# Kernel tuning notes

Measured on AMD Instinct MI355X. Metric: run time of the kernel, lower is better.

The kernel has to match this reference:

```python
import jax, jax.numpy as jnp
import numpy as np

SCORE_THRESH = 0.05
NMS_THRESH = 0.5
MAX_DET = 100
BBOX_XFORM_CLIP = float(np.log(1000.0 / 16.0))


def decode_boxes(proposals, deltas):
    # proposals, deltas: [..., 4] in (x1, y1, x2, y2) / (dx, dy, dw, dh)
    w = proposals[..., 2] - proposals[..., 0]
    h = proposals[..., 3] - proposals[..., 1]
    cx = proposals[..., 0] + 0.5 * w
    cy = proposals[..., 1] + 0.5 * h
    dx, dy = deltas[..., 0], deltas[..., 1]
    dw = jnp.minimum(deltas[..., 2], BBOX_XFORM_CLIP)
    dh = jnp.minimum(deltas[..., 3], BBOX_XFORM_CLIP)
    pcx = dx * w + cx
    pcy = dy * h + cy
    pw = jnp.exp(dw) * w
    ph = jnp.exp(dh) * h
    return jnp.stack([pcx - 0.5 * pw, pcy - 0.5 * ph,
                      pcx + 0.5 * pw, pcy + 0.5 * ph], axis=-1)


def iou_matrix(boxes):
    # boxes: [N, 4] -> [N, N] pairwise IoU
    area = (boxes[:, 2] - boxes[:, 0]) * (boxes[:, 3] - boxes[:, 1])
    lt = jnp.maximum(boxes[:, None, :2], boxes[None, :, :2])
    rb = jnp.minimum(boxes[:, None, 2:], boxes[None, :, 2:])
    wh = jnp.clip(rb - lt, 0.0)
    inter = wh[..., 0] * wh[..., 1]
    union = area[:, None] + area[None, :] - inter
    return inter / (union + 1e-9)


def nms_single(boxes, scores, labels, valid):
    # Greedy batched NMS for one image with fixed shapes.
    N = boxes.shape[0]
    neg = jnp.finfo(scores.dtype).min
    s = jnp.where(valid, scores, neg)
    # class-offset trick (torchvision batched_nms)
    max_coord = jnp.max(jnp.where(valid[:, None], boxes, 0.0))
    obox = boxes + labels.astype(boxes.dtype)[:, None] * (max_coord + 1.0)
    order = jnp.argsort(-s)
    obox_s = obox[order]
    s_s = s[order]
    valid_s = valid[order]
    iou = iou_matrix(obox_s)  # [N, N]
    idxs = jnp.arange(N)

    def body(i, suppressed):
        keep_i = jnp.logical_and(~suppressed[i], valid_s[i])
        return suppressed | (keep_i & (iou[i] > NMS_THRESH) & (idxs > i))

    suppressed = jax.lax.fori_loop(0, N, body, jnp.zeros((N,), bool))
    keep = (~suppressed) & valid_s
    final_s = jnp.where(keep, s_s, neg)
    top_s, top_i = jax.lax.top_k(final_s, MAX_DET)
    sel = order[top_i]
    valid_out = keep[top_i]
    out_boxes = jnp.where(valid_out[:, None], boxes[sel], 0.0)
    out_scores = jnp.where(valid_out, top_s, 0.0)
    out_labels = jnp.where(valid_out, labels[sel], -1)
    return out_boxes, out_scores, out_labels


def setup_inputs() -> dict:
    key = jax.random.key(0)
    k1, k2, k3, k4, k5 = jax.random.split(key, 5)
    B, N, C = 16, 1024, 91
    class_logits = jax.random.normal(k1, (B, N, C), dtype=jnp.float32)
    bbox_deltas = 0.1 * jax.random.normal(k2, (B, N, C * 4), dtype=jnp.float32)
    xy = jax.random.uniform(k3, (B, N, 2), dtype=jnp.float32) * 800.0
    wh = jax.random.uniform(k4, (B, N, 2), dtype=jnp.float32) * 200.0 + 1.0
    roi_proposals = jnp.concatenate([xy, xy + wh], axis=-1)
    image_sizes = jax.random.randint(k5, (B, 2), 512, 1333).astype(jnp.int32)  # (h, w)
    return {"class_logits": class_logits, "bbox_deltas": bbox_deltas,
            "roi_proposals": roi_proposals, "image_sizes": image_sizes}


def reference(class_logits, bbox_deltas, roi_proposals, image_sizes):
    B, N, C = class_logits.shape
    probs_all = jax.nn.softmax(class_logits, axis=-1)
    scores = jnp.max(probs_all, axis=-1)          # [B, N]
    labels = jnp.argmax(probs_all, axis=-1)       # [B, N]
    valid = (labels > 0) & (scores > SCORE_THRESH)
    # gather per-class deltas (same as the 4*idx .. 4*idx+3 gather)
    deltas = bbox_deltas.reshape(B, N, C, 4)
    matched = jnp.take_along_axis(deltas, labels[:, :, None, None], axis=2)[:, :, 0, :]
    boxes = decode_boxes(roi_proposals, matched)
    hw = image_sizes.astype(boxes.dtype)          # (h, w)
    bound = jnp.stack([hw[:, 1], hw[:, 0], hw[:, 1], hw[:, 0]], axis=-1)[:, None, :]
    boxes = jnp.clip(boxes, 0.0, bound)
    out_boxes, out_scores, out_labels = jax.vmap(nms_single)(boxes, scores, labels, valid)
    return out_boxes, out_scores, out_labels
```

## Files before the change

### kernel.cpp

```cpp
#include <hip/hip_runtime.h>
#include <math.h>

#define NN 1024
#define CC 91
#define MAXDET 100
typedef unsigned long long ull;
#define SENT 0xFFFFFFFFFFFFFFFFULL

struct alignas(16) D4 { double x, y, z, w; };

__global__ __launch_bounds__(256) void k1_decode(
    const float* __restrict__ logits, const float* __restrict__ deltas,
    const float* __restrict__ props,  const int* __restrict__ imsz,
    D4* __restrict__ dbox, double* __restrict__ score64,
    int* __restrict__ label, ull* __restrict__ skeyG, ull* __restrict__ keptKey)
{
    int lane = threadIdx.x & 63;
    int wv   = threadIdx.x >> 6;
    int pid  = blockIdx.x * 4 + wv;
    const float* lg = logits + (size_t)pid * CC;

    float v0 = lg[lane];
    float v1 = (lane < CC - 64) ? lg[64 + lane] : -INFINITY;
    float m; int idx;
    if (v0 >= v1) { m = v0; idx = lane; } else { m = v1; idx = 64 + lane; }
    #pragma unroll
    for (int off = 32; off > 0; off >>= 1) {
        float om = __shfl_xor(m, off);
        int   oi = __shfl_xor(idx, off);
        if (om > m || (om == m && oi < idx)) { m = om; idx = oi; }
    }
    double e = exp((double)v0 - (double)m);
    if (lane < CC - 64) e += exp((double)v1 - (double)m);
    #pragma unroll
    for (int off = 32; off > 0; off >>= 1) e += __shfl_xor(e, off);

    if (lane == 0) {
        double score = 1.0 / e;
        int lbl = idx;
        int vld = (lbl > 0 && score > 0.05) ? 1 : 0;
        float4 d = ((const float4*)deltas)[(size_t)pid * CC + lbl];
        float4 p = ((const float4*)props)[pid];
        double w  = (double)p.z - (double)p.x;
        double h  = (double)p.w - (double)p.y;
        double cx = (double)p.x + 0.5 * w;
        double cy = (double)p.y + 0.5 * h;
        const double CLIPV = 4.135166556742356;
        double dw = fmin((double)d.z, CLIPV), dh = fmin((double)d.w, CLIPV);
        double pcx = (double)d.x * w + cx, pcy = (double)d.y * h + cy;
        double pw = exp(dw) * w, ph = exp(dh) * h;
        double x1 = pcx - 0.5 * pw, y1 = pcy - 0.5 * ph;
        double x2 = pcx + 0.5 * pw, y2 = pcy + 0.5 * ph;
        int b = pid >> 10;
        double bw = (double)imsz[b * 2 + 1], bh = (double)imsz[b * 2 + 0];
        x1 = fmin(fmax(x1, 0.0), bw); y1 = fmin(fmax(y1, 0.0), bh);
        x2 = fmin(fmax(x2, 0.0), bw); y2 = fmin(fmax(y2, 0.0), bh);
        dbox[pid]    = D4{x1, y1, x2, y2};
        score64[pid] = score;
        label[pid]   = vld ? lbl : 0;
        double seff = vld ? score : -1e300;
        ull u   = (ull)__double_as_longlong(seff);
        ull asc = (u >> 63) ? ~u : (u | 0x8000000000000000ULL);
        skeyG[pid]   = (~asc & ~1023ULL) | (ull)(pid & 1023);
        keptKey[pid] = SENT;
    }
}

__global__ __launch_bounds__(256) void k2_nms(
    const D4* __restrict__ dbox, const int* __restrict__ label,
    const ull* __restrict__ skeyG, ull* __restrict__ keptKey)
{
    __shared__ int sMemb[4 * 64];
    __shared__ int sPosR[4 * 64];
    __shared__ ull sKeyR[4 * 64];
    int lane = threadIdx.x & 63, wv = threadIdx.x >> 6;
    int gw = blockIdx.x * 4 + wv;
    int b  = gw / 90;
    int c  = 1 + gw % 90;
    int base = b * NN;
    ull lmlt = (lane == 0) ? 0ULL : ((1ULL << lane) - 1ULL);

    int myl[16];
    #pragma unroll
    for (int w = 0; w < 16; ++w) myl[w] = label[base + w * 64 + lane];

    int nmem = 0;
    #pragma unroll
    for (int w = 0; w < 16; ++w) {
        bool match = (myl[w] == c);
        ull mb = __ballot(match);
        if (match) {
            int slot = nmem + (int)__popcll(mb & lmlt);
            if (slot < 64) sMemb[wv * 64 + slot] = w * 64 + lane;
        }
        nmem += (int)__popcll(mb);
        if (nmem >= 64) break;
    }
    int n = nmem < 64 ? nmem : 64;
    if (n == 0) return;

    int p = sMemb[wv * 64 + (lane < n ? lane : 0)];
    ull key = skeyG[base + p];
    int rank = 0;
    for (int j = 0; j < n; ++j) {
        ull kj = __shfl(key, j);
        rank += (int)(kj < key);
    }
    if (lane < n) { sPosR[wv * 64 + rank] = p; sKeyR[wv * 64 + rank] = key; }
    int rl  = wv * 64 + (lane < n ? lane : 0);
    int p2  = sPosR[rl];
    ull k2v = sKeyR[rl];

    D4 bx = dbox[base + p2];
    double ma = (bx.z - bx.x) * (bx.w - bx.y);
    ull pm = 0;
    for (int j = 0; j < n; ++j) {
        double jx = __shfl(bx.x, j), jy = __shfl(bx.y, j);
        double jz = __shfl(bx.z, j), jw = __shfl(bx.w, j);
        double ja = __shfl(ma, j);
        double xx1 = fmax(bx.x, jx), yy1 = fmax(bx.y, jy);
        double xx2 = fmin(bx.z, jz), yy2 = fmin(bx.w, jw);
        double iw = fmax(xx2 - xx1, 0.0), ih = fmax(yy2 - yy1, 0.0);
        double inter = iw * ih;
        bool hit = (inter > 0.5 * (ma + ja - inter + 1e-9)) && (j < lane);
        pm |= ((ull)hit) << j;
    }
    bool act = lane < n;
    ull avail = __ballot(act);
    ull keptw = 0; bool supp = false;
    while (avail) {
        int k0 = __builtin_ctzll(avail);
        keptw |= 1ULL << k0;
        supp = supp || ((pm >> k0) & 1ULL);
        avail &= ~__ballot(supp);
        avail &= ~((2ULL << k0) - 1ULL);
    }
    if (act && ((keptw >> lane) & 1ULL)) keptKey[base + p2] = k2v;
}

__global__ __launch_bounds__(1024) void k3_top(
    const D4* __restrict__ dbox, const double* __restrict__ score64,
    const int* __restrict__ label, const ull* __restrict__ keptKey,
    float* __restrict__ out)
{
    __shared__ ull sRun[NN];
    int b = blockIdx.x, t = threadIdx.x;
    int lane = t & 63, wv = t >> 6;
    int base = b * NN;

    ull key = keptKey[base + t];
    for (int k = 2; k <= 64; k <<= 1)
        for (int j = k >> 1; j > 0; j >>= 1) {
            ull part = __shfl_xor(key, j);
            bool keepMin = ((lane & j) == 0) == ((lane & k) == 0);
            ull mn = key < part ? key : part;
            ull mx = key < part ? part : key;
            key = keepMin ? mn : mx;
        }
    sRun[wv * 64 + lane] = key;
    __syncthreads();

    if (wv < 8) {
        ull a  = sRun[wv * 128 + lane];
        ull bb = sRun[wv * 128 + 64 + lane];
        ull br = __shfl(bb, 63 - lane);
        ull lo = a < br ? a : br;
        ull hi = a < br ? br : a;
        #pragma unroll
        for (int j = 32; j > 0; j >>= 1) {
            bool km = ((lane & j) == 0);
            ull pl = __shfl_xor(lo, j);
            lo = km ? (lo < pl ? lo : pl) : (lo < pl ? pl : lo);
            ull ph = __shfl_xor(hi, j);
            hi = km ? (hi < ph ? hi : ph) : (hi < ph ? ph : hi);
        }
        sRun[wv * 128 + lane] = lo;
        sRun[wv * 128 + 64 + lane] = hi;
    }
    for (int nm = 4; nm >= 1; nm >>= 1) {
        __syncthreads();
        ull Alo = 0, Ahi = 0, Blo = 0, Bhi = 0;
        if (wv < nm) {
            Alo = sRun[wv * 256 + lane];
            Ahi = sRun[wv * 256 + 64 + lane];
            Blo = sRun[wv * 256 + 128 + lane];
            Bhi = sRun[wv * 256 + 192 + lane];
        }
        __syncthreads();
        if (wv < nm) {
            ull rBhi = __shfl(Bhi, 63 - lane);
            ull rBlo = __shfl(Blo, 63 - lane);
            ull Mlo = Alo < rBhi ? Alo : rBhi;
            ull Mhi = Ahi < rBlo ? Ahi : rBlo;
            ull l2 = Mlo < Mhi ? Mlo : Mhi;
            ull h2 = Mlo < Mhi ? Mhi : Mlo;
            #pragma unroll
            for (int j = 32; j > 0; j >>= 1) {
                bool km = ((lane & j) == 0);
                ull pl = __shfl_xor(l2, j);
                l2 = km ? (l2 < pl ? l2 : pl) : (l2 < pl ? pl : l2);
                ull ph = __shfl_xor(h2, j);
                h2 = km ? (h2 < ph ? h2 : ph) : (h2 < ph ? ph : h2);
            }
            sRun[wv * 128 + lane] = l2;
            sRun[wv * 128 + 64 + lane] = h2;
        }
    }
    if (wv == 0) {
        float* oBox   = out;
        float* oScore = out + 6400;
        float* oLabel = out + 8000;
        #pragma unroll
        for (int rsel = 0; rsel < 2; ++rsel) {
            int rank = rsel * 64 + lane;
            if (rank < MAXDET) {
                ull kf = sRun[rsel * 64 + lane];
                int q = b * MAXDET + rank;
                if (kf == SENT) {
                    oBox[q * 4 + 0] = 0.f; oBox[q * 4 + 1] = 0.f;
                    oBox[q * 4 + 2] = 0.f; oBox[q * 4 + 3] = 0.f;
                    oScore[q] = 0.f;
                    oLabel[q] = -1.f;
                } else {
                    int p = (int)(kf & 1023ULL);
                    D4 bx = dbox[base + p];
                    oBox[q * 4 + 0] = (float)bx.x; oBox[q * 4 + 1] = (float)bx.y;
                    oBox[q * 4 + 2] = (float)bx.z; oBox[q * 4 + 3] = (float)bx.w;
                    oScore[q] = (float)score64[base + p];
                    oLabel[q] = (float)label[base + p];
                }
            }
        }
    }
}

extern "C" void kernel_launch(void* const* d_in, const int* in_sizes, int n_in,
                              void* d_out, int out_size, void* d_ws, size_t ws_size,
                              hipStream_t stream) {
    const float* logits = (const float*)d_in[0];
    const float* deltas = (const float*)d_in[1];
    const float* props  = (const float*)d_in[2];
    const int*   imsz   = (const int*)d_in[3];
    char* ws = (char*)d_ws;
    D4*     dbox    = (D4*)(ws + 0);
    double* score64 = (double*)(ws + 524288);
    int*    label   = (int*)(ws + 655360);
    ull*    skeyG   = (ull*)(ws + 720896);
    ull*    keptKey = (ull*)(ws + 851968);
    float* out = (float*)d_out;

    k1_decode<<<dim3(4096), dim3(256), 0, stream>>>(logits, deltas, props, imsz,
                                                    dbox, score64, label, skeyG, keptKey);
    k2_nms<<<dim3(360), dim3(256), 0, stream>>>(dbox, label, skeyG, keptKey);
    k3_top<<<dim3(16), dim3(1024), 0, stream>>>(dbox, score64, label, keptKey, out);
}
```

Before: 99.13 us.

## Fuse decode, per-class NMS and top-k into one cooperative kernel with grid syncs

Replaces the three separate kernel launches with one cooperative kernel of 256 blocks of 1024 threads, separated by grid-wide syncs. The decode phase now has each wave handle four proposals instead of one. The NMS phase maps class-waves across blocks, and the top-k phase runs on the first 16 blocks. The aim is to remove launch overhead and inter-kernel gaps, at the cost of grid-sync latency, larger 1024-thread blocks, and the requirement that all 256 blocks be co-resident.

```diff
diff --git a/kernel.cpp b/kernel.cpp
--- a/kernel.cpp
+++ b/kernel.cpp
@@ -1,5 +1,8 @@
 #include <hip/hip_runtime.h>
+#include <hip/hip_cooperative_groups.h>
 #include <math.h>
+
+namespace cg = cooperative_groups;
 
 #define NN 1024
 #define CC 91
@@ -9,225 +12,229 @@
 
 struct alignas(16) D4 { double x, y, z, w; };
 
-__global__ __launch_bounds__(256) void k1_decode(
+__global__ __launch_bounds__(1024, 4) void fused_all(
     const float* __restrict__ logits, const float* __restrict__ deltas,
     const float* __restrict__ props,  const int* __restrict__ imsz,
     D4* __restrict__ dbox, double* __restrict__ score64,
-    int* __restrict__ label, ull* __restrict__ skeyG, ull* __restrict__ keptKey)
-{
-    int lane = threadIdx.x & 63;
-    int wv   = threadIdx.x >> 6;
-    int pid  = blockIdx.x * 4 + wv;
-    const float* lg = logits + (size_t)pid * CC;
-
-    float v0 = lg[lane];
-    float v1 = (lane < CC - 64) ? lg[64 + lane] : -INFINITY;
-    float m; int idx;
-    if (v0 >= v1) { m = v0; idx = lane; } else { m = v1; idx = 64 + lane; }
-    #pragma unroll
-    for (int off = 32; off > 0; off >>= 1) {
-        float om = __shfl_xor(m, off);
-        int   oi = __shfl_xor(idx, off);
-        if (om > m || (om == m && oi < idx)) { m = om; idx = oi; }
-    }
-    double e = exp((double)v0 - (double)m);
-    if (lane < CC - 64) e += exp((double)v1 - (double)m);
-    #pragma unroll
-    for (int off = 32; off > 0; off >>= 1) e += __shfl_xor(e, off);
-
-    if (lane == 0) {
-        double score = 1.0 / e;
-        int lbl = idx;
-        int vld = (lbl > 0 && score > 0.05) ? 1 : 0;
-        float4 d = ((const float4*)deltas)[(size_t)pid * CC + lbl];
-        float4 p = ((const float4*)props)[pid];
-        double w  = (double)p.z - (double)p.x;
-        double h  = (double)p.w - (double)p.y;
-        double cx = (double)p.x + 0.5 * w;
-        double cy = (double)p.y + 0.5 * h;
-        const double CLIPV = 4.135166556742356;
-        double dw = fmin((double)d.z, CLIPV), dh = fmin((double)d.w, CLIPV);
-        double pcx = (double)d.x * w + cx, pcy = (double)d.y * h + cy;
-        double pw = exp(dw) * w, ph = exp(dh) * h;
-        double x1 = pcx - 0.5 * pw, y1 = pcy - 0.5 * ph;
-        double x2 = pcx + 0.5 * pw, y2 = pcy + 0.5 * ph;
-        int b = pid >> 10;
-        double bw = (double)imsz[b * 2 + 1], bh = (double)imsz[b * 2 + 0];
-        x1 = fmin(fmax(x1, 0.0), bw); y1 = fmin(fmax(y1, 0.0), bh);
-        x2 = fmin(fmax(x2, 0.0), bw); y2 = fmin(fmax(y2, 0.0), bh);
-        dbox[pid]    = D4{x1, y1, x2, y2};
-        score64[pid] = score;
-        label[pid]   = vld ? lbl : 0;
-        double seff = vld ? score : -1e300;
-        ull u   = (ull)__double_as_longlong(seff);
-        ull asc = (u >> 63) ? ~u : (u | 0x8000000000000000ULL);
-        skeyG[pid]   = (~asc & ~1023ULL) | (ull)(pid & 1023);
-        keptKey[pid] = SENT;
-    }
-}
-
-__global__ __launch_bounds__(256) void k2_nms(
-    const D4* __restrict__ dbox, const int* __restrict__ label,
-    const ull* __restrict__ skeyG, ull* __restrict__ keptKey)
-{
-    __shared__ int sMemb[4 * 64];
-    __shared__ int sPosR[4 * 64];
-    __shared__ ull sKeyR[4 * 64];
-    int lane = threadIdx.x & 63, wv = threadIdx.x >> 6;
-    int gw = blockIdx.x * 4 + wv;
-    int b  = gw / 90;
-    int c  = 1 + gw % 90;
-    int base = b * NN;
-    ull lmlt = (lane == 0) ? 0ULL : ((1ULL << lane) - 1ULL);
-
-    int myl[16];
-    #pragma unroll
-    for (int w = 0; w < 16; ++w) myl[w] = label[base + w * 64 + lane];
-
-    int nmem = 0;
-    #pragma unroll
-    for (int w = 0; w < 16; ++w) {
-        bool match = (myl[w] == c);
-        ull mb = __ballot(match);
-        if (match) {
-            int slot = nmem + (int)__popcll(mb & lmlt);
-            if (slot < 64) sMemb[wv * 64 + slot] = w * 64 + lane;
-        }
-        nmem += (int)__popcll(mb);
-        if (nmem >= 64) break;
-    }
-    int n = nmem < 64 ? nmem : 64;
-    if (n == 0) return;
-
-    int p = sMemb[wv * 64 + (lane < n ? lane : 0)];
-    ull key = skeyG[base + p];
-    int rank = 0;
-    for (int j = 0; j < n; ++j) {
-        ull kj = __shfl(key, j);
-        rank += (int)(kj < key);
-    }
-    if (lane < n) { sPosR[wv * 64 + rank] = p; sKeyR[wv * 64 + rank] = key; }
-    int rl  = wv * 64 + (lane < n ? lane : 0);
-    int p2  = sPosR[rl];
-    ull k2v = sKeyR[rl];
-
-    D4 bx = dbox[base + p2];
-    double ma = (bx.z - bx.x) * (bx.w - bx.y);
-    ull pm = 0;
-    for (int j = 0; j < n; ++j) {
-        double jx = __shfl(bx.x, j), jy = __shfl(bx.y, j);
-        double jz = __shfl(bx.z, j), jw = __shfl(bx.w, j);
-        double ja = __shfl(ma, j);
-        double xx1 = fmax(bx.x, jx), yy1 = fmax(bx.y, jy);
-        double xx2 = fmin(bx.z, jz), yy2 = fmin(bx.w, jw);
-        double iw = fmax(xx2 - xx1, 0.0), ih = fmax(yy2 - yy1, 0.0);
-        double inter = iw * ih;
-        bool hit = (inter > 0.5 * (ma + ja - inter + 1e-9)) && (j < lane);
-        pm |= ((ull)hit) << j;
-    }
-    bool act = lane < n;
-    ull avail = __ballot(act);
-    ull keptw = 0; bool supp = false;
-    while (avail) {
-        int k0 = __builtin_ctzll(avail);
-        keptw |= 1ULL << k0;
-        supp = supp || ((pm >> k0) & 1ULL);
-        avail &= ~__ballot(supp);
-        avail &= ~((2ULL << k0) - 1ULL);
-    }
-    if (act && ((keptw >> lane) & 1ULL)) keptKey[base + p2] = k2v;
-}
-
-__global__ __launch_bounds__(1024) void k3_top(
-    const D4* __restrict__ dbox, const double* __restrict__ score64,
-    const int* __restrict__ label, const ull* __restrict__ keptKey,
+    int* __restrict__ label, ull* __restrict__ skeyG, ull* __restrict__ keptKey,
     float* __restrict__ out)
 {
+    __shared__ int sMemb[16 * 64];
+    __shared__ int sPosR[16 * 64];
+    __shared__ ull sKeyR[16 * 64];
     __shared__ ull sRun[NN];
-    int b = blockIdx.x, t = threadIdx.x;
-    int lane = t & 63, wv = t >> 6;
-    int base = b * NN;
-
-    ull key = keptKey[base + t];
-    for (int k = 2; k <= 64; k <<= 1)
-        for (int j = k >> 1; j > 0; j >>= 1) {
-            ull part = __shfl_xor(key, j);
-            bool keepMin = ((lane & j) == 0) == ((lane & k) == 0);
-            ull mn = key < part ? key : part;
-            ull mx = key < part ? part : key;
-            key = keepMin ? mn : mx;
-        }
-    sRun[wv * 64 + lane] = key;
-    __syncthreads();
-
-    if (wv < 8) {
-        ull a  = sRun[wv * 128 + lane];
-        ull bb = sRun[wv * 128 + 64 + lane];
-        ull br = __shfl(bb, 63 - lane);
-        ull lo = a < br ? a : br;
-        ull hi = a < br ? br : a;
+
+    cg::grid_group grid = cg::this_grid();
+    int t = threadIdx.x, lane = t & 63, wv = t >> 6;
+
+    {
+        int gwave = blockIdx.x * 16 + wv;
+        double e_my = 1.0; int idx_my = 0;
         #pragma unroll
-        for (int j = 32; j > 0; j >>= 1) {
-            bool km = ((lane & j) == 0);
-            ull pl = __shfl_xor(lo, j);
-            lo = km ? (lo < pl ? lo : pl) : (lo < pl ? pl : lo);
-            ull ph = __shfl_xor(hi, j);
-            hi = km ? (hi < ph ? hi : ph) : (hi < ph ? ph : hi);
-        }
-        sRun[wv * 128 + lane] = lo;
-        sRun[wv * 128 + 64 + lane] = hi;
+        for (int q = 0; q < 4; ++q) {
+            int pid = gwave * 4 + q;
+            const float* lg = logits + (size_t)pid * CC;
+            float v0 = lg[lane];
+            float v1 = (lane < CC - 64) ? lg[64 + lane] : -INFINITY;
+            float m; int idx;
+            if (v0 >= v1) { m = v0; idx = lane; } else { m = v1; idx = 64 + lane; }
+            #pragma unroll
+            for (int off = 32; off > 0; off >>= 1) {
+                float om = __shfl_xor(m, off);
+                int   oi = __shfl_xor(idx, off);
+                if (om > m || (om == m && oi < idx)) { m = om; idx = oi; }
+            }
+            double e = exp((double)v0 - (double)m) + exp((double)v1 - (double)m);
+            #pragma unroll
+            for (int off = 32; off > 0; off >>= 1) e += __shfl_xor(e, off);
+            if (lane == q) { e_my = e; idx_my = idx; }
+        }
+        if (lane < 4) {
+            int pid = gwave * 4 + lane;
+            double score = 1.0 / e_my;
+            int lbl = idx_my;
+            int vld = (lbl > 0 && score > 0.05) ? 1 : 0;
+            float4 d = ((const float4*)deltas)[(size_t)pid * CC + lbl];
+            float4 p = ((const float4*)props)[pid];
+            double w  = (double)p.z - (double)p.x;
+            double h  = (double)p.w - (double)p.y;
+            double cx = (double)p.x + 0.5 * w;
+            double cy = (double)p.y + 0.5 * h;
+            const double CLIPV = 4.135166556742356;
+            double dw = fmin((double)d.z, CLIPV), dh = fmin((double)d.w, CLIPV);
+            double pcx = (double)d.x * w + cx, pcy = (double)d.y * h + cy;
+            double pw = exp(dw) * w, ph = exp(dh) * h;
+            double x1 = pcx - 0.5 * pw, y1 = pcy - 0.5 * ph;
+            double x2 = pcx + 0.5 * pw, y2 = pcy + 0.5 * ph;
+            int b = pid >> 10;
+            double bw = (double)imsz[b * 2 + 1], bh = (double)imsz[b * 2 + 0];
+            x1 = fmin(fmax(x1, 0.0), bw); y1 = fmin(fmax(y1, 0.0), bh);
+            x2 = fmin(fmax(x2, 0.0), bw); y2 = fmin(fmax(y2, 0.0), bh);
+            dbox[pid]    = D4{x1, y1, x2, y2};
+            score64[pid] = score;
+            label[pid]   = vld ? lbl : 0;
+            double seff = vld ? score : -1e300;
+            ull u   = (ull)__double_as_longlong(seff);
+            ull asc = (u >> 63) ? ~u : (u | 0x8000000000000000ULL);
+            skeyG[pid]   = (~asc & ~1023ULL) | (ull)(pid & 1023);
+            keptKey[pid] = SENT;
+        }
     }
-    for (int nm = 4; nm >= 1; nm >>= 1) {
+    grid.sync();
+
+    {
+        int gw = blockIdx.x + 256 * wv;
+        if (gw < 1440) {
+            int b  = gw / 90;
+            int c  = 1 + gw % 90;
+            int base = b * NN;
+            ull lmlt = (lane == 0) ? 0ULL : ((1ULL << lane) - 1ULL);
+
+            int myl[16];
+            #pragma unroll
+            for (int w = 0; w < 16; ++w) myl[w] = label[base + w * 64 + lane];
+
+            int nmem = 0;
+            #pragma unroll
+            for (int w = 0; w < 16; ++w) {
+                bool match = (myl[w] == c);
+                ull mb = __ballot(match);
+                if (match) {
+                    int slot = nmem + (int)__popcll(mb & lmlt);
+                    if (slot < 64) sMemb[wv * 64 + slot] = w * 64 + lane;
+                }
+                nmem += (int)__popcll(mb);
+                if (nmem >= 64) break;
+            }
+            int n = nmem < 64 ? nmem : 64;
+            if (n > 0) {
+                int p = sMemb[wv * 64 + (lane < n ? lane : 0)];
+                ull key = skeyG[base + p];
+                int rank = 0;
+                for (int j = 0; j < n; ++j) {
+                    ull kj = __shfl(key, j);
+                    rank += (int)(kj < key);
+                }
+                if (lane < n) { sPosR[wv * 64 + rank] = p; sKeyR[wv * 64 + rank] = key; }
+                int rl  = wv * 64 + (lane < n ? lane : 0);
+                int p2  = sPosR[rl];
+                ull k2v = sKeyR[rl];
+
+                D4 bx = dbox[base + p2];
+                double ma = (bx.z - bx.x) * (bx.w - bx.y);
+                ull pm = 0;
+                for (int j = 0; j < n; ++j) {
+                    double jx = __shfl(bx.x, j), jy = __shfl(bx.y, j);
+                    double jz = __shfl(bx.z, j), jw = __shfl(bx.w, j);
+                    double ja = __shfl(ma, j);
+                    double xx1 = fmax(bx.x, jx), yy1 = fmax(bx.y, jy);
+                    double xx2 = fmin(bx.z, jz), yy2 = fmin(bx.w, jw);
+                    double iw = fmax(xx2 - xx1, 0.0), ih = fmax(yy2 - yy1, 0.0);
+                    double inter = iw * ih;
+                    bool hit = (inter > 0.5 * (ma + ja - inter + 1e-9)) && (j < lane);
+                    pm |= ((ull)hit) << j;
+                }
+                bool act = lane < n;
+                ull avail = __ballot(act);
+                ull keptw = 0; bool supp = false;
+                while (avail) {
+                    int k0 = __builtin_ctzll(avail);
+                    keptw |= 1ULL << k0;
+                    supp = supp || ((pm >> k0) & 1ULL);
+                    avail &= ~__ballot(supp);
+                    avail &= ~((2ULL << k0) - 1ULL);
+                }
+                if (act && ((keptw >> lane) & 1ULL)) keptKey[base + p2] = k2v;
+            }
+        }
+    }
+    grid.sync();
+
+    if (blockIdx.x < 16) {
+        int b = blockIdx.x;
+        int base = b * NN;
+
+        ull key = keptKey[base + t];
+        for (int k = 2; k <= 64; k <<= 1)
+            for (int j = k >> 1; j > 0; j >>= 1) {
+                ull part = __shfl_xor(key, j);
+                bool keepMin = ((lane & j) == 0) == ((lane & k) == 0);
+                ull mn = key < part ? key : part;
+                ull mx = key < part ? part : key;
+                key = keepMin ? mn : mx;
+            }
+        sRun[wv * 64 + lane] = key;
         __syncthreads();
-        ull Alo = 0, Ahi = 0, Blo = 0, Bhi = 0;
-        if (wv < nm) {
-            Alo = sRun[wv * 256 + lane];
-            Ahi = sRun[wv * 256 + 64 + lane];
-            Blo = sRun[wv * 256 + 128 + lane];
-            Bhi = sRun[wv * 256 + 192 + lane];
-        }
-        __syncthreads();
-        if (wv < nm) {
-            ull rBhi = __shfl(Bhi, 63 - lane);
-            ull rBlo = __shfl(Blo, 63 - lane);
-            ull Mlo = Alo < rBhi ? Alo : rBhi;
-            ull Mhi = Ahi < rBlo ? Ahi : rBlo;
-            ull l2 = Mlo < Mhi ? Mlo : Mhi;
-            ull h2 = Mlo < Mhi ? Mhi : Mlo;
+
+        if (wv < 8) {
+            ull a  = sRun[wv * 128 + lane];
+            ull bb = sRun[wv * 128 + 64 + lane];
+            ull br = __shfl(bb, 63 - lane);
+            ull lo = a < br ? a : br;
+            ull hi = a < br ? br : a;
             #pragma unroll
             for (int j = 32; j > 0; j >>= 1) {
                 bool km = ((lane & j) == 0);
-                ull pl = __shfl_xor(l2, j);
-                l2 = km ? (l2 < pl ? l2 : pl) : (l2 < pl ? pl : l2);
-                ull ph = __shfl_xor(h2, j);
-                h2 = km ? (h2 < ph ? h2 : ph) : (h2 < ph ? ph : h2);
-            }
-            sRun[wv * 128 + lane] = l2;
-            sRun[wv * 128 + 64 + lane] = h2;
-        }
-    }
-    if (wv == 0) {
-        float* oBox   = out;
-        float* oScore = out + 6400;
-        float* oLabel = out + 8000;
-        #pragma unroll
-        for (int rsel = 0; rsel < 2; ++rsel) {
-            int rank = rsel * 64 + lane;
-            if (rank < MAXDET) {
-                ull kf = sRun[rsel * 64 + lane];
-                int q = b * MAXDET + rank;
-                if (kf == SENT) {
-                    oBox[q * 4 + 0] = 0.f; oBox[q * 4 + 1] = 0.f;
-                    oBox[q * 4 + 2] = 0.f; oBox[q * 4 + 3] = 0.f;
-                    oScore[q] = 0.f;
-                    oLabel[q] = -1.f;
-                } else {
-                    int p = (int)(kf & 1023ULL);
-                    D4 bx = dbox[base + p];
-                    oBox[q * 4 + 0] = (float)bx.x; oBox[q * 4 + 1] = (float)bx.y;
-                    oBox[q * 4 + 2] = (float)bx.z; oBox[q * 4 + 3] = (float)bx.w;
-                    oScore[q] = (float)score64[base + p];
-                    oLabel[q] = (float)label[base + p];
+                ull pl = __shfl_xor(lo, j);
+                lo = km ? (lo < pl ? lo : pl) : (lo < pl ? pl : lo);
+                ull ph = __shfl_xor(hi, j);
+                hi = km ? (hi < ph ? hi : ph) : (hi < ph ? ph : hi);
+            }
+            sRun[wv * 128 + lane] = lo;
+            sRun[wv * 128 + 64 + lane] = hi;
+        }
+        for (int nm = 4; nm >= 1; nm >>= 1) {
+            __syncthreads();
+            ull Alo = 0, Ahi = 0, Blo = 0, Bhi = 0;
+            if (wv < nm) {
+                Alo = sRun[wv * 256 + lane];
+                Ahi = sRun[wv * 256 + 64 + lane];
+                Blo = sRun[wv * 256 + 128 + lane];
+                Bhi = sRun[wv * 256 + 192 + lane];
+            }
+            __syncthreads();
+            if (wv < nm) {
+                ull rBhi = __shfl(Bhi, 63 - lane);
+                ull rBlo = __shfl(Blo, 63 - lane);
+                ull Mlo = Alo < rBhi ? Alo : rBhi;
+                ull Mhi = Ahi < rBlo ? Ahi : rBlo;
+                ull l2 = Mlo < Mhi ? Mlo : Mhi;
+                ull h2 = Mlo < Mhi ? Mhi : Mlo;
+                #pragma unroll
+                for (int j = 32; j > 0; j >>= 1) {
+                    bool km = ((lane & j) == 0);
+                    ull pl = __shfl_xor(l2, j);
+                    l2 = km ? (l2 < pl ? l2 : pl) : (l2 < pl ? pl : l2);
+                    ull ph = __shfl_xor(h2, j);
+                    h2 = km ? (h2 < ph ? h2 : ph) : (h2 < ph ? ph : h2);
+                }
+                sRun[wv * 128 + lane] = l2;
+                sRun[wv * 128 + 64 + lane] = h2;
+            }
+        }
+        if (wv == 0) {
+            float* oBox   = out;
+            float* oScore = out + 6400;
+            float* oLabel = out + 8000;
+            #pragma unroll
+            for (int rsel = 0; rsel < 2; ++rsel) {
+                int rank = rsel * 64 + lane;
+                if (rank < MAXDET) {
+                    ull kf = sRun[rsel * 64 + lane];
+                    int q = b * MAXDET + rank;
+                    if (kf == SENT) {
+                        oBox[q * 4 + 0] = 0.f; oBox[q * 4 + 1] = 0.f;
+                        oBox[q * 4 + 2] = 0.f; oBox[q * 4 + 3] = 0.f;
+                        oScore[q] = 0.f;
+                        oLabel[q] = -1.f;
+                    } else {
+                        int p = (int)(kf & 1023ULL);
+                        D4 bx = dbox[base + p];
+                        oBox[q * 4 + 0] = (float)bx.x; oBox[q * 4 + 1] = (float)bx.y;
+                        oBox[q * 4 + 2] = (float)bx.z; oBox[q * 4 + 3] = (float)bx.w;
+                        oScore[q] = (float)score64[base + p];
+                        oLabel[q] = (float)label[base + p];
+                    }
                 }
             }
         }
@@ -247,10 +254,11 @@
     int*    label   = (int*)(ws + 655360);
     ull*    skeyG   = (ull*)(ws + 720896);
     ull*    keptKey = (ull*)(ws + 851968);
-    float* out = (float*)d_out;
-
-    k1_decode<<<dim3(4096), dim3(256), 0, stream>>>(logits, deltas, props, imsz,
-                                                    dbox, score64, label, skeyG, keptKey);
-    k2_nms<<<dim3(360), dim3(256), 0, stream>>>(dbox, label, skeyG, keptKey);
-    k3_top<<<dim3(16), dim3(1024), 0, stream>>>(dbox, score64, label, keptKey, out);
+    float*  out     = (float*)d_out;
+
+    void* args[] = { (void*)&logits, (void*)&deltas, (void*)&props, (void*)&imsz,
+                     (void*)&dbox, (void*)&score64, (void*)&label, (void*)&skeyG,
+                     (void*)&keptKey, (void*)&out };
+    hipLaunchCooperativeKernel((const void*)fused_all, dim3(256), dim3(1024),
+                               args, 0, stream);
 }
```

New measurement: 160.5 us. 1.62x slower.
